# Performance work log

Measured on AMD Instinct MI355X. Metric: run time of the kernel, lower is better.

Reference implementation:

```python
import jax, jax.numpy as jnp
import numpy as np

# Problem sizes (see shape_source): N points, D embedding dim, B subbatches (events), M labels per event.
N, D, B, M = 2_097_152, 16, 8, 32
DELTA_V, DELTA_D = 0.5, 1.5  # module defaults
EPS = 1e-8


def setup_inputs() -> dict:
    key = jax.random.key(0)
    outputs = jax.random.normal(key, (N, D), dtype=jnp.float32)
    idx = jnp.arange(N)
    # contiguous subbatches, every label present in every subbatch (matches torch.unique structure)
    subbatch_indices = (idx // (N // B)).astype(jnp.int32)
    labels = (idx % M).astype(jnp.int32)
    return {"outputs": outputs, "labels": labels, "subbatch_indices": subbatch_indices}


def reference(outputs, labels, subbatch_indices):
    # normalize=True: L2-normalize each embedding row (note: torch adds eps to the norm, not norm+eps clamp)
    x = outputs / (jnp.linalg.norm(outputs, axis=1) + EPS)[:, None]

    # flat segment id per (subbatch, label) group; every group is populated by construction
    seg = (subbatch_indices * M + labels).astype(jnp.int32)  # [N] in [0, B*M)

    ones = jnp.ones((x.shape[0],), x.dtype)
    counts = jax.ops.segment_sum(ones, seg, num_segments=B * M)        # [B*M] == Nm per group
    mus = jax.ops.segment_sum(x, seg, num_segments=B * M) / counts[:, None]  # [B*M, D] centroids

    # L_pull: per-point hinge on L1 distance to its centroid, weights are all-ones (use_weights=False)
    dist = jnp.sum(jnp.abs(mus[seg] - x), axis=1)                       # [N] L1 distance
    L_pull = jnp.sum(jax.nn.relu(dist - DELTA_V) ** 2 / (M * counts[seg]))

    # L_push: all-pairs centroid hinge within each subbatch, diagonal zeroed
    mus_b = mus.reshape(B, M, D)
    pd = jnp.sum(jnp.abs(mus_b[:, :, None, :] - mus_b[:, None, :, :]), axis=-1)  # [B, M, M]
    hinge = jax.nn.relu(2.0 * DELTA_D - pd) ** 2
    hinge = jnp.where(jnp.eye(M, dtype=bool)[None], 0.0, hinge)
    L_push = jnp.sum(hinge) / (M * (M - 1))

    return (L_pull + L_push) / B
```

## Files before the change

kernel.cpp:

```cpp
#include <hip/hip_runtime.h>
#include <math.h>


#define DD 16
#define MM 32
#define BBATCH 8
#define SEGS 256
#define DELTA_V 0.5f
#define DELTA_D 1.5f
#define NEPS 1e-8f

#define NBLK 1024
#define NTHR 256
#define CHUNKP 2048
#define ITERS (CHUNKP * 4 / NTHR)

#define WS_ZERO_FLOATS 4352

__device__ __forceinline__ void lds_fadd(float* p, float v) {
    __hip_atomic_fetch_add(p, v, __ATOMIC_RELAXED, __HIP_MEMORY_SCOPE_WORKGROUP);
}

__device__ __forceinline__ float block_reduce_sum(float v) {
    #pragma unroll
    for (int o = 32; o > 0; o >>= 1) v += __shfl_down(v, o, 64);
    __shared__ float red[4];
    int wid  = threadIdx.x >> 6;
    int lane = threadIdx.x & 63;
    if (lane == 0) red[wid] = v;
    __syncthreads();
    v = (threadIdx.x < (NTHR >> 6)) ? red[threadIdx.x] : 0.0f;
    if (wid == 0) {
        #pragma unroll
        for (int o = 32; o > 0; o >>= 1) v += __shfl_down(v, o, 64);
    }
    return v;
}

__global__ void __launch_bounds__(NTHR, 8)
k_segsum(const float4* __restrict__ o4,
         const int* __restrict__ labels,
         const int* __restrict__ sub,
         float* __restrict__ seg_sum,
         float* __restrict__ seg_cnt,
         int n) {
    __shared__ float lsT[(DD + 1) * SEGS];
    for (int i = threadIdx.x; i < (DD + 1) * SEGS; i += NTHR) lsT[i] = 0.0f;
    __syncthreads();

    const int tid = threadIdx.x;
    const int j   = tid & 3;
    const int n4  = 4 * n;
    const int qbase = blockIdx.x * (CHUNKP * 4) + tid;

    float4 av = {0.0f, 0.0f, 0.0f, 0.0f};
    float cnt = 0.0f;
    int cur = -1;

    #pragma unroll 4
    for (int it = 0; it < ITERS; ++it) {
        int q = qbase + it * NTHR;
        bool ok = (q < n4);
        int qc = ok ? q : 0;
        float4 v = o4[qc];
        int p = qc >> 2;
        int seg = sub[p] * MM + labels[p];
        float ss = v.x*v.x + v.y*v.y + v.z*v.z + v.w*v.w;
        ss += __shfl_xor(ss, 1, 64);
        ss += __shfl_xor(ss, 2, 64);
        float rn = 1.0f / (sqrtf(ss) + NEPS);
        if (ok) {
            if (seg != cur) {
                if (cur >= 0) {
                    lds_fadd(&lsT[(4*j + 0) * SEGS + cur], av.x);
                    lds_fadd(&lsT[(4*j + 1) * SEGS + cur], av.y);
                    lds_fadd(&lsT[(4*j + 2) * SEGS + cur], av.z);
                    lds_fadd(&lsT[(4*j + 3) * SEGS + cur], av.w);
                    if (j == 0) lds_fadd(&lsT[DD * SEGS + cur], cnt);
                    av = (float4){0.0f, 0.0f, 0.0f, 0.0f};
                    cnt = 0.0f;
                }
                cur = seg;
            }
            av.x += v.x * rn; av.y += v.y * rn;
            av.z += v.z * rn; av.w += v.w * rn;
            cnt += 1.0f;
        }
    }
    if (cur >= 0) {
        lds_fadd(&lsT[(4*j + 0) * SEGS + cur], av.x);
        lds_fadd(&lsT[(4*j + 1) * SEGS + cur], av.y);
        lds_fadd(&lsT[(4*j + 2) * SEGS + cur], av.z);
        lds_fadd(&lsT[(4*j + 3) * SEGS + cur], av.w);
        if (j == 0) lds_fadd(&lsT[DD * SEGS + cur], cnt);
    }
    __syncthreads();
    for (int s = threadIdx.x; s < SEGS; s += NTHR) {
        float c = lsT[DD * SEGS + s];
        if (c != 0.0f) {
            #pragma unroll
            for (int d = 0; d < DD; ++d)
                unsafeAtomicAdd(&seg_sum[s * DD + d], lsT[d * SEGS + s]);
            unsafeAtomicAdd(&seg_cnt[s], c);
        }
    }
}

__global__ void k_finalize_push(float* __restrict__ ws) {
    const float* seg_sum = ws;
    const float* seg_cnt = ws + 4096;
    float* mus  = ws + 4352;
    float* invw = ws + 8448;
    float* push = ws + 8704;

    __shared__ float muT[DD * SEGS];
    int t = threadIdx.x;
    float cnt = seg_cnt[t];
    float ic  = (cnt > 0.0f) ? 1.0f / cnt : 0.0f;
    #pragma unroll
    for (int d = 0; d < DD; ++d) {
        float m = seg_sum[t * DD + d] * ic;
        mus[t * DD + d]   = m;
        muT[d * SEGS + t] = m;
    }
    invw[t] = (cnt > 0.0f) ? 1.0f / ((float)MM * cnt) : 0.0f;
    __syncthreads();

    int b = t >> 5, m1 = t & 31;
    float acc = 0.0f;
    for (int m2 = 0; m2 < MM; ++m2) {
        float pd = 0.0f;
        #pragma unroll
        for (int d = 0; d < DD; ++d)
            pd += fabsf(muT[d * SEGS + b * MM + m1] - muT[d * SEGS + b * MM + m2]);
        float h = 2.0f * DELTA_D - pd;
        if (m2 != m1 && h > 0.0f) acc += h * h;
    }
    float tot = block_reduce_sum(acc);
    if (t == 0) push[0] = tot / (float)(MM * (MM - 1));
}

__global__ void __launch_bounds__(NTHR, 8)
k_pull(const float4* __restrict__ o4,
       const int* __restrict__ labels,
       const int* __restrict__ sub,
       const float* __restrict__ mus,
       const float* __restrict__ invw,
       float* __restrict__ pull_part,
       int n) {
    __shared__ float muL[DD * SEGS];
    __shared__ float siw[SEGS];
    for (int i = threadIdx.x; i < DD * SEGS; i += NTHR) muL[i] = mus[i];
    for (int i = threadIdx.x; i < SEGS; i += NTHR) siw[i] = invw[i];
    __syncthreads();

    const int tid = threadIdx.x;
    const int j   = tid & 3;
    const int n4  = 4 * n;
    const int qbase = blockIdx.x * (CHUNKP * 4) + tid;

    float4 mreg = {0.0f, 0.0f, 0.0f, 0.0f};
    float iw = 0.0f;
    int cur = -1;
    float acc = 0.0f;

    #pragma unroll 4
    for (int it = 0; it < ITERS; ++it) {
        int q = qbase + it * NTHR;
        bool ok = (q < n4);
        int qc = ok ? q : 0;
        float4 v = o4[qc];
        int p = qc >> 2;
        int seg = sub[p] * MM + labels[p];
        float ss = v.x*v.x + v.y*v.y + v.z*v.z + v.w*v.w;
        ss += __shfl_xor(ss, 1, 64);
        ss += __shfl_xor(ss, 2, 64);
        float rn = 1.0f / (sqrtf(ss) + NEPS);
        if (seg != cur) {
            cur = seg;
            mreg = *(const float4*)&muL[seg * DD + 4 * j];
            iw = siw[seg];
        }
        float d4 = fabsf(mreg.x - v.x * rn) + fabsf(mreg.y - v.y * rn)
                 + fabsf(mreg.z - v.z * rn) + fabsf(mreg.w - v.w * rn);
        d4 += __shfl_xor(d4, 1, 64);
        d4 += __shfl_xor(d4, 2, 64);
        if (ok && j == 0) {
            float h = d4 - DELTA_V;
            if (h > 0.0f) acc = fmaf(h * h, iw, acc);
        }
    }
    float tot = block_reduce_sum(acc);
    if (threadIdx.x == 0) pull_part[blockIdx.x] = tot;
}

__global__ void k_final(const float* __restrict__ ws, float* __restrict__ out) {
    const float* push      = ws + 8704;
    const float* pull_part = ws + 8720;
    int t = threadIdx.x;
    float v = 0.0f;
    #pragma unroll
    for (int k = 0; k < NBLK / NTHR; ++k) v += pull_part[t + k * NTHR];
    float tot = block_reduce_sum(v);
    if (t == 0) out[0] = (tot + push[0]) * (1.0f / (float)BBATCH);
}

extern "C" void kernel_launch(void* const* d_in, const int* in_sizes, int n_in,
                              void* d_out, int out_size, void* d_ws, size_t ws_size,
                              hipStream_t stream) {
    const float* outputs = (const float*)d_in[0];
    const int* labels    = (const int*)d_in[1];
    const int* sub       = (const int*)d_in[2];
    int n = in_sizes[0] / DD;

    float* ws        = (float*)d_ws;
    float* seg_sum   = ws;
    float* seg_cnt   = ws + 4096;
    float* mus       = ws + 4352;
    float* invw      = ws + 8448;
    float* pull_part = ws + 8720;

    hipMemsetAsync(d_ws, 0, WS_ZERO_FLOATS * sizeof(float), stream);

    k_segsum<<<NBLK, NTHR, 0, stream>>>((const float4*)outputs, labels, sub,
                                        seg_sum, seg_cnt, n);
    k_finalize_push<<<1, NTHR, 0, stream>>>(ws);
    k_pull<<<NBLK, NTHR, 0, stream>>>((const float4*)outputs, labels, sub,
                                      mus, invw, pull_part, n);
    k_final<<<1, NTHR, 0, stream>>>(ws, (float*)d_out);
}
```

Before: 329.3 us.

## Add uniform-segment fast path with register prefetch pipeline in segsum and pull

```diff
diff --git a/kernel.cpp b/kernel.cpp
--- a/kernel.cpp
+++ b/kernel.cpp
@@ -14,6 +14,7 @@
 #define NTHR 256
 #define CHUNKP 2048
 #define ITERS (CHUNKP * 4 / NTHR)
+#define PIPE 4
 
 #define WS_ZERO_FLOATS 4352
 
@@ -37,7 +38,7 @@
     return v;
 }
 
-__global__ void __launch_bounds__(NTHR, 8)
+__global__ void __launch_bounds__(NTHR, 4)
 k_segsum(const float4* __restrict__ o4,
          const int* __restrict__ labels,
          const int* __restrict__ sub,
@@ -45,7 +46,9 @@
          float* __restrict__ seg_cnt,
          int n) {
     __shared__ float lsT[(DD + 1) * SEGS];
+    __shared__ int bad;
     for (int i = threadIdx.x; i < (DD + 1) * SEGS; i += NTHR) lsT[i] = 0.0f;
+    if (threadIdx.x == 0) bad = 0;
     __syncthreads();
 
     const int tid = threadIdx.x;
@@ -53,46 +56,100 @@
     const int n4  = 4 * n;
     const int qbase = blockIdx.x * (CHUNKP * 4) + tid;
 
+    int qc0 = (qbase < n4) ? qbase : j;
+    int p0  = qc0 >> 2;
+    const int seg0 = sub[p0] * MM + labels[p0];
+
+    float4 vb[PIPE]; int sb[PIPE], lb[PIPE];
+    #pragma unroll
+    for (int k = 0; k < PIPE; ++k) {
+        int q  = qbase + k * NTHR;
+        int qc = (q < n4) ? q : j;
+        vb[k] = o4[qc];
+        int p = qc >> 2;
+        sb[k] = sub[p];
+        lb[k] = labels[p];
+    }
+
     float4 av = {0.0f, 0.0f, 0.0f, 0.0f};
     float cnt = 0.0f;
-    int cur = -1;
-
+    int allok = 1;
     #pragma unroll 4
     for (int it = 0; it < ITERS; ++it) {
+        int k = it & (PIPE - 1);
+        float4 v = vb[k];
+        int seg  = sb[k] * MM + lb[k];
+        {
+            int qn  = qbase + (it + PIPE) * NTHR;
+            int qcn = (qn < n4 && (it + PIPE) < ITERS) ? qn : j;
+            vb[k] = o4[qcn];
+            int pn = qcn >> 2;
+            sb[k] = sub[pn];
+            lb[k] = labels[pn];
+        }
         int q = qbase + it * NTHR;
-        bool ok = (q < n4);
-        int qc = ok ? q : 0;
-        float4 v = o4[qc];
-        int p = qc >> 2;
-        int seg = sub[p] * MM + labels[p];
+        int ok = (q < n4);
         float ss = v.x*v.x + v.y*v.y + v.z*v.z + v.w*v.w;
         ss += __shfl_xor(ss, 1, 64);
         ss += __shfl_xor(ss, 2, 64);
         float rn = 1.0f / (sqrtf(ss) + NEPS);
-        if (ok) {
-            if (seg != cur) {
-                if (cur >= 0) {
-                    lds_fadd(&lsT[(4*j + 0) * SEGS + cur], av.x);
-                    lds_fadd(&lsT[(4*j + 1) * SEGS + cur], av.y);
-                    lds_fadd(&lsT[(4*j + 2) * SEGS + cur], av.z);
-                    lds_fadd(&lsT[(4*j + 3) * SEGS + cur], av.w);
-                    if (j == 0) lds_fadd(&lsT[DD * SEGS + cur], cnt);
-                    av = (float4){0.0f, 0.0f, 0.0f, 0.0f};
-                    cnt = 0.0f;
+        float mk = ok ? 1.0f : 0.0f;
+        rn *= mk;
+        allok &= (!ok) | (seg == seg0);
+        av.x += v.x * rn; av.y += v.y * rn;
+        av.z += v.z * rn; av.w += v.w * rn;
+        cnt += mk;
+    }
+
+    if (!allok) bad = 1;
+    __syncthreads();
+
+    if (bad == 0) {
+        lds_fadd(&lsT[(4*j + 0) * SEGS + seg0], av.x);
+        lds_fadd(&lsT[(4*j + 1) * SEGS + seg0], av.y);
+        lds_fadd(&lsT[(4*j + 2) * SEGS + seg0], av.z);
+        lds_fadd(&lsT[(4*j + 3) * SEGS + seg0], av.w);
+        if (j == 0) lds_fadd(&lsT[DD * SEGS + seg0], cnt);
+    } else {
+        float4 av2 = {0.0f, 0.0f, 0.0f, 0.0f};
+        float cnt2 = 0.0f;
+        int cur = -1;
+        for (int it = 0; it < ITERS; ++it) {
+            int q = qbase + it * NTHR;
+            bool ok = (q < n4);
+            int qc = ok ? q : j;
+            float4 v = o4[qc];
+            int p = qc >> 2;
+            int seg = sub[p] * MM + labels[p];
+            float ss = v.x*v.x + v.y*v.y + v.z*v.z + v.w*v.w;
+            ss += __shfl_xor(ss, 1, 64);
+            ss += __shfl_xor(ss, 2, 64);
+            float rn = 1.0f / (sqrtf(ss) + NEPS);
+            if (ok) {
+                if (seg != cur) {
+                    if (cur >= 0) {
+                        lds_fadd(&lsT[(4*j + 0) * SEGS + cur], av2.x);
+                        lds_fadd(&lsT[(4*j + 1) * SEGS + cur], av2.y);
+                        lds_fadd(&lsT[(4*j + 2) * SEGS + cur], av2.z);
+                        lds_fadd(&lsT[(4*j + 3) * SEGS + cur], av2.w);
+                        if (j == 0) lds_fadd(&lsT[DD * SEGS + cur], cnt2);
+                        av2 = (float4){0.0f, 0.0f, 0.0f, 0.0f};
+                        cnt2 = 0.0f;
+                    }
+                    cur = seg;
                 }
-                cur = seg;
+                av2.x += v.x * rn; av2.y += v.y * rn;
+                av2.z += v.z * rn; av2.w += v.w * rn;
+                cnt2 += 1.0f;
             }
-            av.x += v.x * rn; av.y += v.y * rn;
-            av.z += v.z * rn; av.w += v.w * rn;
-            cnt += 1.0f;
-        }
-    }
-    if (cur >= 0) {
-        lds_fadd(&lsT[(4*j + 0) * SEGS + cur], av.x);
-        lds_fadd(&lsT[(4*j + 1) * SEGS + cur], av.y);
-        lds_fadd(&lsT[(4*j + 2) * SEGS + cur], av.z);
-        lds_fadd(&lsT[(4*j + 3) * SEGS + cur], av.w);
-        if (j == 0) lds_fadd(&lsT[DD * SEGS + cur], cnt);
+        }
+        if (cur >= 0) {
+            lds_fadd(&lsT[(4*j + 0) * SEGS + cur], av2.x);
+            lds_fadd(&lsT[(4*j + 1) * SEGS + cur], av2.y);
+            lds_fadd(&lsT[(4*j + 2) * SEGS + cur], av2.z);
+            lds_fadd(&lsT[(4*j + 3) * SEGS + cur], av2.w);
+            if (j == 0) lds_fadd(&lsT[DD * SEGS + cur], cnt2);
+        }
     }
     __syncthreads();
     for (int s = threadIdx.x; s < SEGS; s += NTHR) {
@@ -140,7 +197,7 @@
     if (t == 0) push[0] = tot / (float)(MM * (MM - 1));
 }
 
-__global__ void __launch_bounds__(NTHR, 8)
+__global__ void __launch_bounds__(NTHR, 4)
 k_pull(const float4* __restrict__ o4,
        const int* __restrict__ labels,
        const int* __restrict__ sub,
@@ -150,8 +207,10 @@
        int n) {
     __shared__ float muL[DD * SEGS];
     __shared__ float siw[SEGS];
+    __shared__ int bad;
     for (int i = threadIdx.x; i < DD * SEGS; i += NTHR) muL[i] = mus[i];
     for (int i = threadIdx.x; i < SEGS; i += NTHR) siw[i] = invw[i];
+    if (threadIdx.x == 0) bad = 0;
     __syncthreads();
 
     const int tid = threadIdx.x;
@@ -159,35 +218,80 @@
     const int n4  = 4 * n;
     const int qbase = blockIdx.x * (CHUNKP * 4) + tid;
 
-    float4 mreg = {0.0f, 0.0f, 0.0f, 0.0f};
-    float iw = 0.0f;
-    int cur = -1;
-    float acc = 0.0f;
-
+    int qc0 = (qbase < n4) ? qbase : j;
+    int p0  = qc0 >> 2;
+    const int seg0 = sub[p0] * MM + labels[p0];
+    const float4 mreg = *(const float4*)&muL[seg0 * DD + 4 * j];
+    const float iw0 = siw[seg0] * ((j == 0) ? 1.0f : 0.0f);
+
+    float4 vb[PIPE]; int sb[PIPE], lb[PIPE];
+    #pragma unroll
+    for (int k = 0; k < PIPE; ++k) {
+        int q  = qbase + k * NTHR;
+        int qc = (q < n4) ? q : j;
+        vb[k] = o4[qc];
+        int p = qc >> 2;
+        sb[k] = sub[p];
+        lb[k] = labels[p];
+    }
+
+    float accF = 0.0f;
+    int allok = 1;
     #pragma unroll 4
     for (int it = 0; it < ITERS; ++it) {
+        int k = it & (PIPE - 1);
+        float4 v = vb[k];
+        int seg  = sb[k] * MM + lb[k];
+        {
+            int qn  = qbase + (it + PIPE) * NTHR;
+            int qcn = (qn < n4 && (it + PIPE) < ITERS) ? qn : j;
+            vb[k] = o4[qcn];
+            int pn = qcn >> 2;
+            sb[k] = sub[pn];
+            lb[k] = labels[pn];
+        }
         int q = qbase + it * NTHR;
-        bool ok = (q < n4);
-        int qc = ok ? q : 0;
-        float4 v = o4[qc];
-        int p = qc >> 2;
-        int seg = sub[p] * MM + labels[p];
+        int ok = (q < n4);
         float ss = v.x*v.x + v.y*v.y + v.z*v.z + v.w*v.w;
         ss += __shfl_xor(ss, 1, 64);
         ss += __shfl_xor(ss, 2, 64);
         float rn = 1.0f / (sqrtf(ss) + NEPS);
-        if (seg != cur) {
-            cur = seg;
-            mreg = *(const float4*)&muL[seg * DD + 4 * j];
-            iw = siw[seg];
-        }
+        allok &= (!ok) | (seg == seg0);
         float d4 = fabsf(mreg.x - v.x * rn) + fabsf(mreg.y - v.y * rn)
                  + fabsf(mreg.z - v.z * rn) + fabsf(mreg.w - v.w * rn);
         d4 += __shfl_xor(d4, 1, 64);
         d4 += __shfl_xor(d4, 2, 64);
-        if (ok && j == 0) {
-            float h = d4 - DELTA_V;
-            if (h > 0.0f) acc = fmaf(h * h, iw, acc);
+        float h  = fmaxf(d4 - DELTA_V, 0.0f);
+        float mk = ok ? 1.0f : 0.0f;
+        accF = fmaf(h * h * mk, iw0, accF);
+    }
+
+    if (!allok) bad = 1;
+    __syncthreads();
+
+    float acc = accF;
+    if (bad != 0) {
+        acc = 0.0f;
+        for (int it = 0; it < ITERS; ++it) {
+            int q = qbase + it * NTHR;
+            bool ok = (q < n4);
+            int qc = ok ? q : j;
+            float4 v = o4[qc];
+            int p = qc >> 2;
+            int seg = sub[p] * MM + labels[p];
+            float ss = v.x*v.x + v.y*v.y + v.z*v.z + v.w*v.w;
+            ss += __shfl_xor(ss, 1, 64);
+            ss += __shfl_xor(ss, 2, 64);
+            float rn = 1.0f / (sqrtf(ss) + NEPS);
+            const float4 m = *(const float4*)&muL[seg * DD + 4 * j];
+            float d4 = fabsf(m.x - v.x * rn) + fabsf(m.y - v.y * rn)
+                     + fabsf(m.z - v.z * rn) + fabsf(m.w - v.w * rn);
+            d4 += __shfl_xor(d4, 1, 64);
+            d4 += __shfl_xor(d4, 2, 64);
+            if (ok && j == 0) {
+                float h = d4 - DELTA_V;
+                if (h > 0.0f) acc = fmaf(h * h, siw[seg], acc);
+            }
         }
     }
     float tot = block_reduce_sum(acc);
```

Result: no change. 334.0 us (+1.4%).
